# Performance work log

Hardware: AMD Instinct MI355X
Metric: run time of the kernel (lower is better)

Reference implementation:

```python
import jax, jax.numpy as jnp
import numpy as np

D_MODEL = 1024
NUM_HEADS = 16
HEAD_DIM = D_MODEL // NUM_HEADS


def setup_inputs() -> dict:
    key = jax.random.key(0)
    k_x, k_wqkv, k_bqkv, k_wo, k_bo = jax.random.split(key, 5)
    B, T = 4, 2048
    s = 1.0 / np.sqrt(D_MODEL)
    return {
        "x": jax.random.normal(k_x, (B, T, D_MODEL), dtype=jnp.float32),
        "w_qkv": jax.random.uniform(k_wqkv, (D_MODEL, 3 * D_MODEL), jnp.float32, -s, s),
        "b_qkv": jax.random.uniform(k_bqkv, (3 * D_MODEL,), jnp.float32, -s, s),
        "w_out": jax.random.uniform(k_wo, (D_MODEL, D_MODEL), jnp.float32, -s, s),
        "b_out": jax.random.uniform(k_bo, (D_MODEL,), jnp.float32, -s, s),
    }


def reference(x, w_qkv, b_qkv, w_out, b_out):
    B, T, _ = x.shape
    H, Dh = NUM_HEADS, HEAD_DIM
    scale = Dh ** -0.5
    qkv = x @ w_qkv + b_qkv                       # [B,T,3D]
    qkv = qkv.reshape(B, T, 3, H, Dh)
    q = jnp.transpose(qkv[:, :, 0], (0, 2, 1, 3))  # [B,H,T,Dh]
    k = jnp.transpose(qkv[:, :, 1], (0, 2, 1, 3))
    v = jnp.transpose(qkv[:, :, 2], (0, 2, 1, 3))
    scores = jnp.einsum('bhqd,bhkd->bhqk', q, k) * scale
    causal = jnp.tril(jnp.ones((T, T), dtype=bool))
    scores = jnp.where(causal, scores, -jnp.inf)
    w = jax.nn.softmax(scores, axis=-1)
    out = jnp.einsum('bhqk,bhkd->bhqd', w, v)     # [B,H,T,Dh]
    out = jnp.transpose(out, (0, 2, 1, 3)).reshape(B, T, H * Dh)
    return out @ w_out + b_out
```

## Files before the change

kernel.cpp:

```cpp
#include <hip/hip_runtime.h>

typedef unsigned short u16;
typedef unsigned u32;
typedef float f32x4 __attribute__((ext_vector_type(4)));
typedef __bf16 bf16x8 __attribute__((ext_vector_type(8)));
typedef __bf16 bf16x2 __attribute__((ext_vector_type(2)));
typedef u32 u32x4 __attribute__((ext_vector_type(4)));
typedef u16 u16x4 __attribute__((ext_vector_type(4)));
typedef int i32x2 __attribute__((ext_vector_type(2)));

#define MFMA_16x16x32(a, b, c) __builtin_amdgcn_mfma_f32_16x16x32_bf16((a), (b), (c), 0, 0, 0)

#if __has_builtin(__builtin_amdgcn_exp2f)
#define EXP2(x) __builtin_amdgcn_exp2f(x)
#else
#define EXP2(x) exp2f(x)
#endif


__device__ __forceinline__ u16 f2bf(float f) {
  unsigned u = __builtin_bit_cast(unsigned, f);
  unsigned r = ((u >> 16) & 1u) + 0x7FFFu;
  return (u16)((u + r) >> 16);
}

__device__ __forceinline__ u32 pk2(float x, float y) {
  bf16x2 v = {(__bf16)x, (__bf16)y};
  return __builtin_bit_cast(u32, v);
}

__device__ __forceinline__ void gload16(const void* g, void* l) {
  __builtin_amdgcn_global_load_lds(
      (const __attribute__((address_space(1))) void*)g,
      (__attribute__((address_space(3))) void*)l, 16, 0, 0);
}



__global__ void cvt_to_bf16(const float* __restrict__ in, u16* __restrict__ out, int n) {
  const int s = blockIdx.x * 256 + threadIdx.x;
  if (s * 8 >= n) return;
  const int l = s & 63, f = (s >> 6) & 7, kb = (s >> 9) & 31, R = s >> 14;
  const int rr = ((f >> 2) << 6) + ((f & 3) << 4) + (l & 15);
  const int row = (R << 7) + rr;
  const int k = (kb << 5) + ((l >> 4) << 3);
  const float* src = in + (size_t)row * 1024 + k;
  const f32x4 a = *(const f32x4*)src;
  const f32x4 b = *(const f32x4*)(src + 4);
  u16x4 u0, u1;
#pragma unroll
  for (int j = 0; j < 4; ++j) { u0[j] = f2bf(a[j]); u1[j] = f2bf(b[j]); }
  *(u16x4*)(out + (size_t)s * 8) = u0;
  *(u16x4*)(out + (size_t)s * 8 + 4) = u1;
}

__global__ void transpose_cvt(const float* __restrict__ in, u16* __restrict__ out,
                              int rows, int cols) {
  __shared__ float t[64][65];
  const int rb = blockIdx.y * 64, cb = blockIdx.x * 64;
  for (int i = threadIdx.x; i < 4096; i += 256) {
    const int r = i >> 6, c = i & 63;
    t[r][c] = in[(size_t)(rb + r) * cols + cb + c];
  }
  __syncthreads();
  for (int u = threadIdx.x; u < 512; u += 256) {
    const int c = u >> 3, k8 = u & 7;
    const int nrow = cb + c;
    const int kg = rb + k8 * 8;
    const int R = nrow >> 7, rr = nrow & 127;
    const int fB = ((rr >> 6) << 2) + ((rr >> 4) & 3);
    const int kb = kg >> 5, koct = (kg >> 3) & 3;
    u16* dst = out + (((size_t)R * 32 + kb) * 8 + fB) * 512 + ((koct << 4) + (rr & 15)) * 8;
    u16x4 u0, u1;
#pragma unroll
    for (int j = 0; j < 4; ++j) {
      u0[j] = f2bf(t[k8 * 8 + j][c]);
      u1[j] = f2bf(t[k8 * 8 + 4 + j][c]);
    }
    *(u16x4*)dst = u0;
    *(u16x4*)(dst + 4) = u1;
  }
}

template <int EPI>
__global__ __launch_bounds__(256, 4) void gemm_bt(
    const u16* __restrict__ A, const u16* __restrict__ Bt, int K,
    const float* __restrict__ bias,
    u16* __restrict__ oq, u16* __restrict__ ok, u16* __restrict__ ov,
    float* __restrict__ of, int N, int nbx) {
  __shared__ __align__(16) u16 As[2][4096];
  __shared__ __align__(16) u16 Bs[2][4096];
  const int tid = threadIdx.x;
  const int lane = tid & 63, w = tid >> 6;
  const int g = lane >> 4, cc = lane & 15;
  const int wr = w >> 1, wc = w & 1;

  const int cpx = gridDim.x >> 3;
  const int bid = ((int)blockIdx.x & 7) * cpx + ((int)blockIdx.x >> 3);
  const int bx = bid % nbx, by = bid / nbx;

  const u16* pa = A + ((size_t)by * 256 + w) * 512 + lane * 8;
  const u16* pb = Bt + ((size_t)bx * 256 + w) * 512 + lane * 8;

  f32x4 acc[4][4] = {};

#define STG(S, T)                                              \
  do {                                                         \
    const size_t o_ = (size_t)(T) * 4096;                      \
    gload16(pa + o_, &As[S][w * 512 + lane * 8]);              \
    gload16(pa + o_ + 2048, &As[S][(w + 4) * 512 + lane * 8]); \
    gload16(pb + o_, &Bs[S][w * 512 + lane * 8]);              \
    gload16(pb + o_ + 2048, &Bs[S][(w + 4) * 512 + lane * 8]); \
  } while (0)

#define CMP(S, DOSTG, T)                                                 \
  do {                                                                   \
    bf16x8 af[4], bf[4];                                                 \
    _Pragma("unroll") for (int mi = 0; mi < 4; ++mi)                     \
        af[mi] = *(const bf16x8*)&As[S][(wr * 4 + mi) * 512 + lane * 8]; \
    _Pragma("unroll") for (int ni = 0; ni < 4; ++ni)                     \
        bf[ni] = *(const bf16x8*)&Bs[S][(wc * 4 + ni) * 512 + lane * 8]; \
    if (DOSTG) STG(S ^ 1, T);                                            \
    __builtin_amdgcn_s_setprio(1);                                       \
    _Pragma("unroll") for (int mi = 0; mi < 4; ++mi)                     \
      _Pragma("unroll") for (int ni = 0; ni < 4; ++ni)                   \
          acc[mi][ni] = MFMA_16x16x32(af[mi], bf[ni], acc[mi][ni]);      \
    __builtin_amdgcn_s_setprio(0);                                       \
  } while (0)

  STG(0, 0);
  __syncthreads();

  const int np = (K >> 5) >> 1;
  for (int p = 0; p < np - 1; ++p) {
    CMP(0, true, 2 * p + 1);
    __syncthreads();
    CMP(1, true, 2 * p + 2);
    __syncthreads();
  }
  CMP(0, true, 2 * np - 1);
  __syncthreads();
  CMP(1, false, 0);

#undef STG
#undef CMP

  const int m00 = by * 128 + wr * 64 + 4 * g;
  const int n00 = bx * 128 + wc * 64;
#pragma unroll
  for (int ni = 0; ni < 4; ++ni) {
    const int n = n00 + ni * 16 + cc;
    const float bn = bias[n];
    if constexpr (EPI == 0) {
      const int which = n >> 10;
      const int d = n & 1023;
      const int h = d >> 6, dh = d & 63;
      const int dcf = dh >> 5, gf = (dh >> 3) & 3, e = dh & 7;
      const int niv = dh >> 4, ccv = dh & 15;
#pragma unroll
      for (int mi = 0; mi < 4; ++mi) {
        const int mb = m00 + mi * 16;
        const int b = mb >> 11, t0b = mb & 2047;
        const int bh2 = b * 16 + h;
        const int kt = t0b >> 7, tr = t0b & 127;
        if (which == 2) {
          const int kk0 = (tr & ~12) | ((tr & 4) << 1) | ((tr & 8) >> 1);
          const int ko = kk0 >> 5, gv = (kk0 >> 3) & 3, ev = kk0 & 7;
          u16x4 pk;
#pragma unroll
          for (int r = 0; r < 4; ++r) pk[r] = f2bf(acc[mi][ni][r] + bn);
          *(u16x4*)&ov[(((size_t)bh2 * 16 + kt) * 16 + ko * 4 + niv) * 512 +
                       ((gv << 4) + ccv) * 8 + ev] = pk;
        } else if (which == 1) {
          const int ki = tr >> 4;
          u16* dst = ok + (((size_t)bh2 * 16 + kt) * 16 + dcf * 8 + ki) * 512 +
                     ((gf << 4) + (tr & 15)) * 8 + e;
#pragma unroll
          for (int r = 0; r < 4; ++r) dst[r * 8] = f2bf(acc[mi][ni][r] + bn);
        } else {
          const int wf = tr >> 5, mif = (tr >> 4) & 1;
          u16* dst = oq + (((size_t)bh2 * 16 + kt) * 16 + wf * 4 + mif * 2 + dcf) * 512 +
                     ((gf << 4) + (tr & 15)) * 8 + e;
#pragma unroll
          for (int r = 0; r < 4; ++r) dst[r * 8] = f2bf(acc[mi][ni][r] + bn);
        }
      }
    } else {
#pragma unroll
      for (int mi = 0; mi < 4; ++mi) {
        const int m = m00 + mi * 16;
#pragma unroll
        for (int r = 0; r < 4; ++r) of[(size_t)(m + r) * N + n] = acc[mi][ni][r] + bn;
      }
    }
  }
}

__global__ __launch_bounds__(256, 3) void flash_attn(
    const u16* __restrict__ Qb, const u16* __restrict__ Kb,
    const u16* __restrict__ Vt, u16* __restrict__ Ob) {
  __shared__ __align__(16) u16 Ks[8192];
  __shared__ __align__(16) u16 Vs[8192];

  const int bid = blockIdx.x;
  const int tq4 = bid >> 6, t0 = tq4 & 3, ti = tq4 >> 2;
  const int qt = (ti == 0) ? 15 - t0 : (ti == 1) ? 8 + t0 : (ti == 2) ? 7 - t0 : t0;
  const int bh = bid & 63;
  const int tid = threadIdx.x;
  const int lane = tid & 63, w = tid >> 6;
  const int g = lane >> 4, cc = lane & 15;
  const int q0 = qt * 128 + w * 32;

  bf16x8 bq[2][2];
  {
    const u16* qp = Qb + (((size_t)bh * 16 + qt) * 16 + w * 4) * 512 + lane * 8;
#pragma unroll
    for (int mi = 0; mi < 2; ++mi)
#pragma unroll
      for (int dc = 0; dc < 2; ++dc)
        bq[mi][dc] = *(const bf16x8*)(qp + (mi * 2 + dc) * 512);
  }

  const char* kp = (const char*)Kb + (size_t)bh * 262144 + w * 1024 + lane * 16;
  const char* vp = (const char*)Vt + (size_t)bh * 262144 + w * 1024 + lane * 16;
  u16* kl[4];
  u16* vl[4];
#pragma unroll
  for (int i = 0; i < 4; ++i) {
    kl[i] = &Ks[(i * 4 + w) * 512 + lane * 8];
    vl[i] = &Vs[(i * 4 + w) * 512 + lane * 8];
  }
  const u16* krd = &Ks[lane * 8];
  const u16* vrd = &Vs[lane * 8];

  const u32x4 ones_u = {0x3F803F80u, 0x3F803F80u, 0x3F803F80u, 0x3F803F80u};
  const bf16x8 ones = __builtin_bit_cast(bf16x8, ones_u);

  f32x4 acc[2][4] = {};
  f32x4 lsum[2] = {};
  float m_run[2] = {-1e30f, -1e30f};
  const float sc = 0.18033688011112042f;

  u32x4 kreg[4], vreg[4];
#pragma unroll
  for (int i = 0; i < 4; ++i) {
    kreg[i] = *(const u32x4*)(kp + i * 4096);
    vreg[i] = *(const u32x4*)(vp + i * 4096);
  }
  kp += 16384;
  vp += 16384;

  for (int kt = 0; kt <= qt; ++kt) {
    __syncthreads();
#pragma unroll
    for (int i = 0; i < 4; ++i) {
      *(u32x4*)kl[i] = kreg[i];
      *(u32x4*)vl[i] = vreg[i];
    }
    if (kt < qt) {
#pragma unroll
      for (int i = 0; i < 4; ++i) {
        kreg[i] = *(const u32x4*)(kp + i * 4096);
        vreg[i] = *(const u32x4*)(vp + i * 4096);
      }
      kp += 16384;
      vp += 16384;
    }
    __syncthreads();

#pragma unroll
    for (int mi = 0; mi < 2; ++mi) {
      f32x4 s[8] = {};
      __builtin_amdgcn_s_setprio(1);
#pragma unroll
      for (int dc = 0; dc < 2; ++dc) {
        const bf16x8 qf = bq[mi][dc];
#pragma unroll
        for (int ki = 0; ki < 8; ++ki) {
          const bf16x8 ak = *(const bf16x8*)(krd + (dc * 8 + ki) * 512);
          s[ki] = MFMA_16x16x32(ak, qf, s[ki]);
        }
      }
      __builtin_amdgcn_s_setprio(0);

      if (kt == qt) {
        const int qq = w * 32 + mi * 16 + cc;
#pragma unroll
        for (int ki = 0; ki < 8; ++ki) {
          const int kb_ = ki * 16 + 4 * g;
#pragma unroll
          for (int r = 0; r < 4; ++r)
            if (kb_ + r > qq) s[ki][r] = -1e30f;
        }
      }

      float t4[8];
#pragma unroll
      for (int ki = 0; ki < 8; ++ki)
        t4[ki] = fmaxf(fmaxf(s[ki][0], s[ki][1]), fmaxf(s[ki][2], s[ki][3]));
      float mx = fmaxf(fmaxf(fmaxf(t4[0], t4[1]), fmaxf(t4[2], t4[3])),
                       fmaxf(fmaxf(t4[4], t4[5]), fmaxf(t4[6], t4[7])));
      mx = fmaxf(mx, __shfl_xor(mx, 16));
      mx = fmaxf(mx, __shfl_xor(mx, 32));
      const float pm = mx * sc;

      if (!__all(pm - m_run[mi] <= 8.f)) {
        const float mn = fmaxf(m_run[mi], pm);
        const float sf = EXP2(m_run[mi] - mn);
        m_run[mi] = mn;
        float sfr[4];
#pragma unroll
        for (int r = 0; r < 4; ++r) sfr[r] = __shfl(sf, (lane & 48) + 4 * g + r);
#pragma unroll
        for (int r = 0; r < 4; ++r) lsum[mi][r] *= sfr[r];
#pragma unroll
        for (int ni = 0; ni < 4; ++ni)
#pragma unroll
          for (int r = 0; r < 4; ++r) acc[mi][ni][r] *= sfr[r];
      }
      const float mcur = m_run[mi];

#pragma unroll
      for (int ko = 0; ko < 4; ++ko) {
        f32x4 pe, po;
#pragma unroll
        for (int r = 0; r < 4; ++r) {
          pe[r] = EXP2(__builtin_fmaf(s[2 * ko][r], sc, -mcur));
          po[r] = EXP2(__builtin_fmaf(s[2 * ko + 1][r], sc, -mcur));
        }
        const u32 aw = pk2(pe[0], pe[1]), bw2 = pk2(pe[2], pe[3]);
        const u32 cw = pk2(po[0], po[1]), dw = pk2(po[2], po[3]);
#if __has_builtin(__builtin_amdgcn_permlane32_swap)
        const i32x2 s1 = __builtin_amdgcn_permlane32_swap((int)aw, (int)cw, false, false);
        const i32x2 s2 = __builtin_amdgcn_permlane32_swap((int)bw2, (int)dw, false, false);
        const u32x4 wv = {(u32)s1[0], (u32)s2[0], (u32)s1[1], (u32)s2[1]};
#else
        const bool lo2 = (g < 2);
        const u32 r_ac = __shfl_xor(lo2 ? cw : aw, 32);
        const u32 r_bd = __shfl_xor(lo2 ? dw : bw2, 32);
        const u32x4 wv = {lo2 ? aw : r_ac, lo2 ? bw2 : r_bd,
                          lo2 ? r_ac : cw, lo2 ? r_bd : dw};
#endif
        const bf16x8 pf = __builtin_bit_cast(bf16x8, wv);
        __builtin_amdgcn_s_setprio(1);
#pragma unroll
        for (int ni = 0; ni < 4; ++ni) {
          const bf16x8 bv = *(const bf16x8*)(vrd + (ko * 4 + ni) * 512);
          acc[mi][ni] = MFMA_16x16x32(pf, bv, acc[mi][ni]);
        }
        lsum[mi] = MFMA_16x16x32(pf, ones, lsum[mi]);
        __builtin_amdgcn_s_setprio(0);
      }
    }
  }

  const int b = bh >> 4, h = bh & 15;
#pragma unroll
  for (int mi = 0; mi < 2; ++mi) {
    f32x4 inv;
#pragma unroll
    for (int r = 0; r < 4; ++r) inv[r] = 1.f / lsum[mi][r];
#pragma unroll
    for (int ni = 0; ni < 4; ++ni) {
      const int d = h * 64 + ni * 16 + cc;
      const int kbA = d >> 5, koA = (d >> 3) & 3, eA = d & 7;
#pragma unroll
      for (int r = 0; r < 4; ++r) {
        const int tq = q0 + mi * 16 + 4 * g + r;
        const int row = b * 2048 + tq;
        const int R = row >> 7, rr = row & 127;
        const int fA = ((rr >> 6) << 2) + ((rr >> 4) & 3);
        Ob[(((size_t)R * 32 + kbA) * 8 + fA) * 512 + ((koA << 4) + (rr & 15)) * 8 + eA] =
            f2bf(acc[mi][ni][r] * inv[r]);
      }
    }
  }
}


extern "C" void kernel_launch(void* const* d_in, const int* in_sizes, int n_in,
                              void* d_out, int out_size, void* d_ws, size_t ws_size,
                              hipStream_t stream) {
  const float* x     = (const float*)d_in[0];
  const float* w_qkv = (const float*)d_in[1];
  const float* b_qkv = (const float*)d_in[2];
  const float* w_out = (const float*)d_in[3];
  const float* b_out = (const float*)d_in[4];
  float* out = (float*)d_out;
  char* ws = (char*)d_ws;

  u16* xb    = (u16*)(ws + 0);
  u16* wqkvT = (u16*)(ws + 16777216);
  u16* woutT = (u16*)(ws + 23068672);
  u16* qbuf  = (u16*)(ws + 25165824);
  u16* kbuf  = (u16*)(ws + 41943040);
  u16* vbuf  = (u16*)(ws + 58720256);

  cvt_to_bf16<<<4096, 256, 0, stream>>>(x, xb, 8388608);
  transpose_cvt<<<dim3(48, 16), 256, 0, stream>>>(w_qkv, wqkvT, 1024, 3072);
  transpose_cvt<<<dim3(16, 16), 256, 0, stream>>>(w_out, woutT, 1024, 1024);
  gemm_bt<0><<<24 * 64, 256, 0, stream>>>(xb, wqkvT, 1024, b_qkv,
                                          qbuf, kbuf, vbuf, nullptr, 3072, 24);
  flash_attn<<<1024, 256, 0, stream>>>(qbuf, kbuf, vbuf, xb);
  gemm_bt<1><<<8 * 64, 256, 0, stream>>>(xb, woutT, 1024, b_out,
                                         nullptr, nullptr, nullptr, out, 1024, 8);
}
```

Baseline: 157.4 us.

## Double-buffer K/V tiles in LDS and interleave QK^T for both row blocks

```diff
diff --git a/kernel.cpp b/kernel.cpp
--- a/kernel.cpp
+++ b/kernel.cpp
@@ -196,11 +196,11 @@
   }
 }
 
-__global__ __launch_bounds__(256, 3) void flash_attn(
+__global__ __launch_bounds__(256, 2) void flash_attn(
     const u16* __restrict__ Qb, const u16* __restrict__ Kb,
     const u16* __restrict__ Vt, u16* __restrict__ Ob) {
-  __shared__ __align__(16) u16 Ks[8192];
-  __shared__ __align__(16) u16 Vs[8192];
+  __shared__ __align__(16) u16 Ks[2][8192];
+  __shared__ __align__(16) u16 Vs[2][8192];
 
   const int bid = blockIdx.x;
   const int tq4 = bid >> 6, t0 = tq4 & 3, ti = tq4 >> 2;
@@ -210,6 +210,7 @@
   const int lane = tid & 63, w = tid >> 6;
   const int g = lane >> 4, cc = lane & 15;
   const int q0 = qt * 128 + w * 32;
+  const int qq0 = w * 32 + cc, qq1 = w * 32 + 16 + cc;
 
   bf16x8 bq[2][2];
   {
@@ -223,22 +224,13 @@
 
   const char* kp = (const char*)Kb + (size_t)bh * 262144 + w * 1024 + lane * 16;
   const char* vp = (const char*)Vt + (size_t)bh * 262144 + w * 1024 + lane * 16;
-  u16* kl[4];
-  u16* vl[4];
-#pragma unroll
-  for (int i = 0; i < 4; ++i) {
-    kl[i] = &Ks[(i * 4 + w) * 512 + lane * 8];
-    vl[i] = &Vs[(i * 4 + w) * 512 + lane * 8];
-  }
-  const u16* krd = &Ks[lane * 8];
-  const u16* vrd = &Vs[lane * 8];
 
   const u32x4 ones_u = {0x3F803F80u, 0x3F803F80u, 0x3F803F80u, 0x3F803F80u};
   const bf16x8 ones = __builtin_bit_cast(bf16x8, ones_u);
 
-  f32x4 acc[2][4] = {};
-  f32x4 lsum[2] = {};
-  float m_run[2] = {-1e30f, -1e30f};
+  f32x4 ac0[4] = {}, ac1[4] = {};
+  f32x4 ls0 = {}, ls1 = {};
+  float m0 = -1e30f, m1 = -1e30f;
   const float sc = 0.18033688011112042f;
 
   u32x4 kreg[4], vreg[4];
@@ -249,117 +241,121 @@
   }
   kp += 16384;
   vp += 16384;
-
-  for (int kt = 0; kt <= qt; ++kt) {
-    __syncthreads();
-#pragma unroll
-    for (int i = 0; i < 4; ++i) {
-      *(u32x4*)kl[i] = kreg[i];
-      *(u32x4*)vl[i] = vreg[i];
-    }
-    if (kt < qt) {
-#pragma unroll
-      for (int i = 0; i < 4; ++i) {
-        kreg[i] = *(const u32x4*)(kp + i * 4096);
-        vreg[i] = *(const u32x4*)(vp + i * 4096);
-      }
-      kp += 16384;
-      vp += 16384;
-    }
-    __syncthreads();
-
-#pragma unroll
-    for (int mi = 0; mi < 2; ++mi) {
-      f32x4 s[8] = {};
-      __builtin_amdgcn_s_setprio(1);
-#pragma unroll
-      for (int dc = 0; dc < 2; ++dc) {
-        const bf16x8 qf = bq[mi][dc];
-#pragma unroll
-        for (int ki = 0; ki < 8; ++ki) {
-          const bf16x8 ak = *(const bf16x8*)(krd + (dc * 8 + ki) * 512);
-          s[ki] = MFMA_16x16x32(ak, qf, s[ki]);
-        }
-      }
-      __builtin_amdgcn_s_setprio(0);
-
-      if (kt == qt) {
-        const int qq = w * 32 + mi * 16 + cc;
-#pragma unroll
-        for (int ki = 0; ki < 8; ++ki) {
-          const int kb_ = ki * 16 + 4 * g;
-#pragma unroll
-          for (int r = 0; r < 4; ++r)
-            if (kb_ + r > qq) s[ki][r] = -1e30f;
-        }
-      }
-
-      float t4[8];
-#pragma unroll
-      for (int ki = 0; ki < 8; ++ki)
-        t4[ki] = fmaxf(fmaxf(s[ki][0], s[ki][1]), fmaxf(s[ki][2], s[ki][3]));
-      float mx = fmaxf(fmaxf(fmaxf(t4[0], t4[1]), fmaxf(t4[2], t4[3])),
-                       fmaxf(fmaxf(t4[4], t4[5]), fmaxf(t4[6], t4[7])));
-      mx = fmaxf(mx, __shfl_xor(mx, 16));
-      mx = fmaxf(mx, __shfl_xor(mx, 32));
-      const float pm = mx * sc;
-
-      if (!__all(pm - m_run[mi] <= 8.f)) {
-        const float mn = fmaxf(m_run[mi], pm);
-        const float sf = EXP2(m_run[mi] - mn);
-        m_run[mi] = mn;
-        float sfr[4];
-#pragma unroll
-        for (int r = 0; r < 4; ++r) sfr[r] = __shfl(sf, (lane & 48) + 4 * g + r);
-#pragma unroll
-        for (int r = 0; r < 4; ++r) lsum[mi][r] *= sfr[r];
-#pragma unroll
-        for (int ni = 0; ni < 4; ++ni)
-#pragma unroll
-          for (int r = 0; r < 4; ++r) acc[mi][ni][r] *= sfr[r];
-      }
-      const float mcur = m_run[mi];
-
-#pragma unroll
-      for (int ko = 0; ko < 4; ++ko) {
-        f32x4 pe, po;
-#pragma unroll
-        for (int r = 0; r < 4; ++r) {
-          pe[r] = EXP2(__builtin_fmaf(s[2 * ko][r], sc, -mcur));
-          po[r] = EXP2(__builtin_fmaf(s[2 * ko + 1][r], sc, -mcur));
-        }
-        const u32 aw = pk2(pe[0], pe[1]), bw2 = pk2(pe[2], pe[3]);
-        const u32 cw = pk2(po[0], po[1]), dw = pk2(po[2], po[3]);
-#if __has_builtin(__builtin_amdgcn_permlane32_swap)
-        const i32x2 s1 = __builtin_amdgcn_permlane32_swap((int)aw, (int)cw, false, false);
-        const i32x2 s2 = __builtin_amdgcn_permlane32_swap((int)bw2, (int)dw, false, false);
-        const u32x4 wv = {(u32)s1[0], (u32)s2[0], (u32)s1[1], (u32)s2[1]};
-#else
-        const bool lo2 = (g < 2);
-        const u32 r_ac = __shfl_xor(lo2 ? cw : aw, 32);
-        const u32 r_bd = __shfl_xor(lo2 ? dw : bw2, 32);
-        const u32x4 wv = {lo2 ? aw : r_ac, lo2 ? bw2 : r_bd,
-                          lo2 ? r_ac : cw, lo2 ? r_bd : dw};
-#endif
-        const bf16x8 pf = __builtin_bit_cast(bf16x8, wv);
-        __builtin_amdgcn_s_setprio(1);
-#pragma unroll
-        for (int ni = 0; ni < 4; ++ni) {
-          const bf16x8 bv = *(const bf16x8*)(vrd + (ko * 4 + ni) * 512);
-          acc[mi][ni] = MFMA_16x16x32(pf, bv, acc[mi][ni]);
-        }
-        lsum[mi] = MFMA_16x16x32(pf, ones, lsum[mi]);
-        __builtin_amdgcn_s_setprio(0);
-      }
-    }
-  }
+#pragma unroll
+  for (int i = 0; i < 4; ++i) {
+    *(u32x4*)&Ks[0][(i * 4 + w) * 512 + lane * 8] = kreg[i];
+    *(u32x4*)&Vs[0][(i * 4 + w) * 512 + lane * 8] = vreg[i];
+  }
+  __syncthreads();
+
+#define SMPV(S, MR, LS, AC, B)                                              \
+  do {                                                                      \
+    float t4[8];                                                            \
+    _Pragma("unroll") for (int ki = 0; ki < 8; ++ki)                        \
+        t4[ki] = fmaxf(fmaxf(S[ki][0], S[ki][1]), fmaxf(S[ki][2], S[ki][3])); \
+    float mx = fmaxf(fmaxf(fmaxf(t4[0], t4[1]), fmaxf(t4[2], t4[3])),       \
+                     fmaxf(fmaxf(t4[4], t4[5]), fmaxf(t4[6], t4[7])));      \
+    mx = fmaxf(mx, __shfl_xor(mx, 16));                                     \
+    mx = fmaxf(mx, __shfl_xor(mx, 32));                                     \
+    const float pm = mx * sc;                                               \
+    if (!__all(pm - MR <= 8.f)) {                                           \
+      const float mn = fmaxf(MR, pm);                                       \
+      const float sf = EXP2(MR - mn);                                       \
+      MR = mn;                                                              \
+      float sfr[4];                                                        \
+      _Pragma("unroll") for (int r = 0; r < 4; ++r)                         \
+          sfr[r] = __shfl(sf, (lane & 48) + 4 * g + r);                     \
+      _Pragma("unroll") for (int r = 0; r < 4; ++r) LS[r] *= sfr[r];        \
+      _Pragma("unroll") for (int ni = 0; ni < 4; ++ni)                      \
+        _Pragma("unroll") for (int r = 0; r < 4; ++r) AC[ni][r] *= sfr[r];  \
+    }                                                                       \
+    const float mcur = MR;                                                  \
+    _Pragma("unroll") for (int ko = 0; ko < 4; ++ko) {                      \
+      f32x4 pe, po;                                                         \
+      _Pragma("unroll") for (int r = 0; r < 4; ++r) {                       \
+        pe[r] = EXP2(__builtin_fmaf(S[2 * ko][r], sc, -mcur));              \
+        po[r] = EXP2(__builtin_fmaf(S[2 * ko + 1][r], sc, -mcur));          \
+      }                                                                     \
+      const u32 aw = pk2(pe[0], pe[1]), bw2 = pk2(pe[2], pe[3]);            \
+      const u32 cw = pk2(po[0], po[1]), dw = pk2(po[2], po[3]);             \
+      const i32x2 s1_ = __builtin_amdgcn_permlane32_swap((int)aw, (int)cw, false, false); \
+      const i32x2 s2_ = __builtin_amdgcn_permlane32_swap((int)bw2, (int)dw, false, false); \
+      const u32x4 wv = {(u32)s1_[0], (u32)s2_[0], (u32)s1_[1], (u32)s2_[1]}; \
+      const bf16x8 pf = __builtin_bit_cast(bf16x8, wv);                     \
+      __builtin_amdgcn_s_setprio(1);                                        \
+      _Pragma("unroll") for (int ni = 0; ni < 4; ++ni) {                    \
+        const bf16x8 bv = *(const bf16x8*)&Vs[B][(ko * 4 + ni) * 512 + lane * 8]; \
+        AC[ni] = MFMA_16x16x32(pf, bv, AC[ni]);                             \
+      }                                                                     \
+      LS = MFMA_16x16x32(pf, ones, LS);                                     \
+      __builtin_amdgcn_s_setprio(0);                                        \
+    }                                                                       \
+  } while (0)
+
+#define COMPUTE(B, KT)                                                      \
+  do {                                                                      \
+    f32x4 s0[8] = {}, s1[8] = {};                                           \
+    __builtin_amdgcn_s_setprio(1);                                          \
+    _Pragma("unroll") for (int dc = 0; dc < 2; ++dc) {                      \
+      _Pragma("unroll") for (int ki = 0; ki < 8; ++ki) {                    \
+        const bf16x8 ak =                                                   \
+            *(const bf16x8*)&Ks[B][(dc * 8 + ki) * 512 + lane * 8];         \
+        s0[ki] = MFMA_16x16x32(ak, bq[0][dc], s0[ki]);                      \
+        s1[ki] = MFMA_16x16x32(ak, bq[1][dc], s1[ki]);                      \
+      }                                                                     \
+    }                                                                       \
+    __builtin_amdgcn_s_setprio(0);                                          \
+    if ((KT) == qt) {                                                       \
+      _Pragma("unroll") for (int ki = 0; ki < 8; ++ki) {                    \
+        const int kb_ = ki * 16 + 4 * g;                                    \
+        _Pragma("unroll") for (int r = 0; r < 4; ++r) {                     \
+          if (kb_ + r > qq0) s0[ki][r] = -1e30f;                            \
+          if (kb_ + r > qq1) s1[ki][r] = -1e30f;                            \
+        }                                                                   \
+      }                                                                     \
+    }                                                                       \
+    SMPV(s0, m0, ls0, ac0, B);                                              \
+    SMPV(s1, m1, ls1, ac1, B);                                              \
+  } while (0)
+
+#define ITER(KT, B)                                                         \
+  do {                                                                      \
+    const bool pf_ = (KT) < qt;                                             \
+    if (pf_) {                                                              \
+      _Pragma("unroll") for (int i = 0; i < 4; ++i) {                       \
+        kreg[i] = *(const u32x4*)(kp + i * 4096);                           \
+        vreg[i] = *(const u32x4*)(vp + i * 4096);                           \
+      }                                                                     \
+      kp += 16384;                                                          \
+      vp += 16384;                                                          \
+    }                                                                       \
+    COMPUTE(B, KT);                                                         \
+    if (pf_) {                                                              \
+      _Pragma("unroll") for (int i = 0; i < 4; ++i) {                       \
+        *(u32x4*)&Ks[(B) ^ 1][(i * 4 + w) * 512 + lane * 8] = kreg[i];      \
+        *(u32x4*)&Vs[(B) ^ 1][(i * 4 + w) * 512 + lane * 8] = vreg[i];      \
+      }                                                                     \
+    }                                                                       \
+    __syncthreads();                                                        \
+  } while (0)
+
+  int kt = 0;
+  while (kt + 1 <= qt) {
+    ITER(kt, 0);
+    ITER(kt + 1, 1);
+    kt += 2;
+  }
+  if (kt <= qt) ITER(kt, 0);
+
+#undef ITER
+#undef COMPUTE
+#undef SMPV
 
   const int b = bh >> 4, h = bh & 15;
-#pragma unroll
-  for (int mi = 0; mi < 2; ++mi) {
+  auto epi = [&](const f32x4(&AC)[4], const f32x4& LS, int mi) {
     f32x4 inv;
 #pragma unroll
-    for (int r = 0; r < 4; ++r) inv[r] = 1.f / lsum[mi][r];
+    for (int r = 0; r < 4; ++r) inv[r] = 1.f / LS[r];
 #pragma unroll
     for (int ni = 0; ni < 4; ++ni) {
       const int d = h * 64 + ni * 16 + cc;
@@ -371,10 +367,12 @@
         const int R = row >> 7, rr = row & 127;
         const int fA = ((rr >> 6) << 2) + ((rr >> 4) & 3);
         Ob[(((size_t)R * 32 + kbA) * 8 + fA) * 512 + ((koA << 4) + (rr & 15)) * 8 + eA] =
-            f2bf(acc[mi][ni][r] * inv[r]);
+            f2bf(AC[ni][r] * inv[r]);
       }
     }
-  }
+  };
+  epi(ac0, ls0, 0);
+  epi(ac1, ls1, 1);
 }
 
 
```

After: 161.8 us. +2.8%, slower.
